# Kernel tuning notes

Measured on AMD Instinct MI355X. Metric: run time of the kernel, lower is better.

The kernel has to match this reference:

```python
import jax, jax.numpy as jnp
import numpy as np
import math

B, L, D = 8, 2048, 256


def setup_inputs() -> dict:
    key = jax.random.key(0)
    ks = jax.random.split(key, 8)
    return {
        "query": jax.random.normal(ks[0], (B, L, D), dtype=jnp.float32),
        "key": jax.random.normal(ks[1], (B, L, D), dtype=jnp.float32),
        "value": jax.random.normal(ks[2], (B, L, D), dtype=jnp.float32),
        "mask": jax.random.randint(ks[3], (B, L), 0, 2, dtype=jnp.int32),
        "Wq_w": jax.random.normal(ks[4], (D, D), dtype=jnp.float32) * 0.05,
        "Wq_b": jax.random.normal(ks[5], (D,), dtype=jnp.float32) * 0.05,
        "Wk_w": jax.random.normal(ks[6], (D, D), dtype=jnp.float32) * 0.05,
        "Wk_b": jax.random.normal(ks[7], (D,), dtype=jnp.float32) * 0.05,
    }


def reference(query, key, value, mask, Wq_w, Wq_b, Wk_w, Wk_b):
    d = query.shape[-1]
    q = query @ Wq_w.T + Wq_b            # [B, Lq, D]
    k = key @ Wk_w.T + Wk_b              # [B, Lk, D]
    scores = jnp.einsum("bqd,bkd->bqk", q, k) / math.sqrt(d)  # [B, Lq, Lk]
    m = mask.astype(scores.dtype)[:, None, :]                  # [B, 1, Lk]
    # multiplicative then additive masking, as in original
    scores = jnp.where(m == 0, jnp.asarray(-1e9, scores.dtype), scores * m)
    attn = jax.nn.softmax(scores, axis=-1)
    return jnp.einsum("bqk,bkd->bqd", attn, value)
```

## Files before the change

### kernel.cpp

```cpp
#include <hip/hip_runtime.h>
#include <stdint.h>
#include <stddef.h>

#define B_ 8
#define L_ 2048
#define D_ 256
#define KSPLIT 4
#define KRANGE 512
#define KTILE 32
#define NITER 16
#define PSS 40

typedef __bf16 bf16x8 __attribute__((ext_vector_type(8)));
typedef float floatx4 __attribute__((ext_vector_type(4)));
typedef _Float16 half4_t __attribute__((ext_vector_type(4)));

__device__ __forceinline__ short f2bf(float f) {
    union { float f; uint32_t u; } v; v.f = f;
    return (short)((v.u + 0x8000u) >> 16);
}

__device__ __forceinline__ uint32_t pack2bf(float a, float b) {
    union { float f; uint32_t u; } x, y; x.f = a; y.f = b;
    return ((x.u + 0x8000u) >> 16) | ((y.u + 0x8000u) & 0xFFFF0000u);
}

__device__ __forceinline__ void async16(const void* g, void* l) {
    __builtin_amdgcn_global_load_lds(
        (__attribute__((address_space(1))) void*)g,
        (__attribute__((address_space(3))) void*)l,
        16, 0, 0);
}

__global__ __launch_bounds__(256, 3) void proj_kernel(
    const float* __restrict__ Xq, const float* __restrict__ Xk,
    const float* __restrict__ Wq, const float* __restrict__ Wk,
    const float* __restrict__ bq, const float* __restrict__ bk,
    short* __restrict__ Oq, short* __restrict__ Ok)
{
    const float* X    = blockIdx.y ? Xk : Xq;
    const float* W    = blockIdx.y ? Wk : Wq;
    const float* bias = blockIdx.y ? bk : bq;
    short* Out        = blockIdx.y ? Ok : Oq;

    __shared__ uint32_t As[2][64 * 20];
    __shared__ uint32_t Ws[2][256 * 20];

    const int tid  = threadIdx.x;
    const int wid  = tid >> 6;
    const int lane = tid & 63;
    const int m16  = lane & 15;
    const int quad = lane >> 4;
    const int row0 = blockIdx.x * 64;
    const int ar = tid >> 2, cg = tid & 3;

    floatx4 acc[16];
    const floatx4 z4 = {0.f, 0.f, 0.f, 0.f};
#pragma unroll
    for (int i = 0; i < 16; i++) acc[i] = z4;

    {
        const float* srcA = X + (size_t)(row0 + ar) * D_ + cg * 8;
        float4 a = *(const float4*)srcA, b2 = *(const float4*)(srcA + 4);
        uint4 u; u.x = pack2bf(a.x, a.y); u.y = pack2bf(a.z, a.w);
        u.z = pack2bf(b2.x, b2.y); u.w = pack2bf(b2.z, b2.w);
        *(uint4*)&As[0][ar * 20 + cg * 4] = u;
#pragma unroll
        for (int p = 0; p < 4; p++) {
            const float* srcW = W + (size_t)(p * 64 + ar) * D_ + cg * 8;
            float4 wa = *(const float4*)srcW, wb = *(const float4*)(srcW + 4);
            uint4 w; w.x = pack2bf(wa.x, wa.y); w.y = pack2bf(wa.z, wa.w);
            w.z = pack2bf(wb.x, wb.y); w.w = pack2bf(wb.z, wb.w);
            *(uint4*)&Ws[0][(p * 64 + ar) * 20 + cg * 4] = w;
        }
    }
    __syncthreads();

    for (int kc = 0; kc < 8; kc++) {
        const int buf = kc & 1;
        float4 na, nb, nwa[4], nwb[4];
        if (kc < 7) {
            const int k1 = (kc + 1) * 32;
            const float* srcA = X + (size_t)(row0 + ar) * D_ + k1 + cg * 8;
            na = *(const float4*)srcA; nb = *(const float4*)(srcA + 4);
#pragma unroll
            for (int p = 0; p < 4; p++) {
                const float* srcW = W + (size_t)(p * 64 + ar) * D_ + k1 + cg * 8;
                nwa[p] = *(const float4*)srcW; nwb[p] = *(const float4*)(srcW + 4);
            }
        }
        bf16x8 af = *(const bf16x8*)&As[buf][(wid * 16 + m16) * 20 + quad * 4];
#pragma unroll
        for (int n = 0; n < 16; n++) {
            bf16x8 bfr = *(const bf16x8*)&Ws[buf][(n * 16 + m16) * 20 + quad * 4];
            acc[n] = __builtin_amdgcn_mfma_f32_16x16x32_bf16(af, bfr, acc[n], 0, 0, 0);
        }
        if (kc < 7) {
            uint4 u; u.x = pack2bf(na.x, na.y); u.y = pack2bf(na.z, na.w);
            u.z = pack2bf(nb.x, nb.y); u.w = pack2bf(nb.z, nb.w);
            *(uint4*)&As[buf ^ 1][ar * 20 + cg * 4] = u;
#pragma unroll
            for (int p = 0; p < 4; p++) {
                uint4 w; w.x = pack2bf(nwa[p].x, nwa[p].y); w.y = pack2bf(nwa[p].z, nwa[p].w);
                w.z = pack2bf(nwb[p].x, nwb[p].y); w.w = pack2bf(nwb[p].z, nwb[p].w);
                *(uint4*)&Ws[buf ^ 1][(p * 64 + ar) * 20 + cg * 4] = w;
            }
        }
        __syncthreads();
    }
#pragma unroll
    for (int n = 0; n < 16; n++) {
        const int col = n * 16 + m16;
        const float bv = bias[col];
#pragma unroll
        for (int r = 0; r < 4; r++) {
            const int row = row0 + wid * 16 + quad * 4 + r;
            Out[(size_t)row * D_ + col] = f2bf(acc[n][r] + bv);
        }
    }
}

__global__ __launch_bounds__(256, 2) void vtrans_kernel(
    const float* __restrict__ V, short* __restrict__ Vt)
{
    __shared__ uint32_t T[256 * 20];
    const int tid = threadIdx.x;
    const int b  = blockIdx.y;
    const int l0 = blockIdx.x * 32;
    const int r2 = tid >> 4;
    const int dg = tid & 15;
    const int lp = r2 ^ ((dg & 3) << 2);
#pragma unroll
    for (int p = 0; p < 4; p++) {
        int d0 = (dg + p * 16) * 4;
        const float* src = V + ((size_t)b * L_ + l0 + r2 * 2) * D_ + d0;
        float4 e0 = *(const float4*)src;
        float4 e1 = *(const float4*)(src + D_);
        T[(d0 + 0) * 20 + lp] = pack2bf(e0.x, e1.x);
        T[(d0 + 1) * 20 + lp] = pack2bf(e0.y, e1.y);
        T[(d0 + 2) * 20 + lp] = pack2bf(e0.z, e1.z);
        T[(d0 + 3) * 20 + lp] = pack2bf(e0.w, e1.w);
    }
    __syncthreads();
#pragma unroll
    for (int p = 0; p < 4; p++) {
        int d = (tid >> 2) + p * 64;
        int c = tid & 3;
        int cp = c ^ ((d >> 2) & 3);
        uint4 u = *(const uint4*)&T[d * 20 + cp * 4];
        *(uint4*)(Vt + ((size_t)b * D_ + d) * L_ + l0 + c * 8) = u;
    }
}

__global__ __launch_bounds__(256, 2) void flash_kernel(
    const short* __restrict__ Qb, const short* __restrict__ Kb,
    const short* __restrict__ Vt, const int* __restrict__ mask,
    float* __restrict__ Out, _Float16* __restrict__ Part,
    float* __restrict__ Lpart)
{
    __shared__ short Ks[2][KTILE * 256];
    __shared__ short Vs[2][256 * KTILE];
    __shared__ short Ps[4 * 32 * PSS];

    const int tid  = threadIdx.x;
    const int wid  = tid >> 6;
    const int lane = tid & 63;
    const int m16  = lane & 15;
    const int quad = lane >> 4;
    const int b  = blockIdx.x;
    const int q0 = blockIdx.y * 128;
    const int z  = blockIdx.z;

    const short* kbase = Kb + ((size_t)b * L_ + z * KRANGE) * D_;
    const short* vbase = Vt + (size_t)b * D_ * L_;
    const int*   mg    = mask + b * L_ + z * KRANGE;

    bf16x8 qf[2][8];
    {
        const short* qrow = Qb + ((size_t)b * L_ + q0 + wid * 32) * D_;
#pragma unroll
        for (int s2 = 0; s2 < 2; s2++)
#pragma unroll
            for (int kk = 0; kk < 8; kk++)
                qf[s2][kk] = *(const bf16x8*)(qrow + (size_t)(s2 * 16 + m16) * D_ + kk * 32 + quad * 8);
    }

    floatx4 o[2][16];
    const floatx4 z4 = {0.f, 0.f, 0.f, 0.f};
#pragma unroll
    for (int s2 = 0; s2 < 2; s2++)
#pragma unroll
        for (int n = 0; n < 16; n++) o[s2][n] = z4;
    float rsum[2][4] = {{0.f,0.f,0.f,0.f},{0.f,0.f,0.f,0.f}};

    auto stageK = [&](int t, int bufi) {
        short* kl = &Ks[bufi][0];
#pragma unroll
        for (int c = 0; c < 4; c++) {
            int unit = wid * 4 + c;
            int row = unit * 2 + (lane >> 5);
            int g = (lane & 31) ^ (row & 7);
            async16(kbase + (size_t)(t * KTILE + row) * D_ + g * 8, kl + unit * 512);
        }
    };
    auto stageV = [&](int t, int bufi) {
        short* vl = &Vs[bufi][0];
#pragma unroll
        for (int c = 0; c < 4; c++) {
            int unit = wid * 4 + c;
            int d = unit * 16 + (lane >> 2);
            int g = (lane & 3) ^ ((lane >> 2) & 3);
            async16(vbase + (size_t)d * L_ + z * KRANGE + t * KTILE + g * 8, vl + unit * 512);
        }
    };

    stageK(0, 0);
    __builtin_amdgcn_s_waitcnt(0x0F70);
    __syncthreads();

    short* ps = Ps + wid * (32 * PSS);
    const float C2 = 0.09016844f;
    bf16x8 pf0, pf1;

    for (int t = 0; t < NITER; t++) {
        const int buf = t & 1;
        if (t + 1 < NITER) stageK(t + 1, buf ^ 1);
        stageV(t, buf);
        const short* kl = &Ks[buf][0];

        int mv0 = mg[t * KTILE + m16];
        int mv1 = mg[t * KTILE + 16 + m16];

        floatx4 sA[2][2];
#pragma unroll
        for (int s2 = 0; s2 < 2; s2++) { sA[s2][0] = z4; sA[s2][1] = z4; }
#pragma unroll
        for (int kk = 0; kk < 8; kk++) {
#pragma unroll
            for (int j = 0; j < 2; j++) {
                int row = j * 16 + m16;
                int cidx = (kk * 4 + quad) ^ (m16 & 7);
                bf16x8 kf = *(const bf16x8*)(kl + row * 256 + cidx * 8);
                sA[0][j] = __builtin_amdgcn_mfma_f32_16x16x32_bf16(qf[0][kk], kf, sA[0][j], 0, 0, 0);
                sA[1][j] = __builtin_amdgcn_mfma_f32_16x16x32_bf16(qf[1][kk], kf, sA[1][j], 0, 0, 0);
            }
        }

        if (t > 0) {
            const short* vl = &Vs[buf ^ 1][0];
#pragma unroll
            for (int n = 0; n < 16; n++) {
                int rowd = n * 16 + m16;
                int cidx = quad ^ (m16 & 3);
                bf16x8 vf = *(const bf16x8*)(vl + rowd * 32 + cidx * 8);
                o[0][n] = __builtin_amdgcn_mfma_f32_16x16x32_bf16(pf0, vf, o[0][n], 0, 0, 0);
                o[1][n] = __builtin_amdgcn_mfma_f32_16x16x32_bf16(pf1, vf, o[1][n], 0, 0, 0);
            }
        }

        float moff0 = mv0 ? 0.f : -1.0e30f;
        float moff1 = mv1 ? 0.f : -1.0e30f;
#pragma unroll
        for (int s2 = 0; s2 < 2; s2++) {
#pragma unroll
            for (int j = 0; j < 2; j++) {
                const float moff = j ? moff1 : moff0;
#pragma unroll
                for (int r = 0; r < 4; r++) {
                    float p = exp2f(fmaf(sA[s2][j][r], C2, moff));
                    rsum[s2][r] += p;
                    ps[(s2 * 16 + quad * 4 + r) * PSS + j * 16 + m16] = f2bf(p);
                }
            }
        }
        __builtin_amdgcn_s_waitcnt(0xC07F);
        pf0 = *(const bf16x8*)(ps + (size_t)m16 * PSS + quad * 8);
        pf1 = *(const bf16x8*)(ps + (size_t)(16 + m16) * PSS + quad * 8);

        __builtin_amdgcn_s_waitcnt(0x0F70);
        __syncthreads();
    }

    {
        const short* vl = &Vs[(NITER - 1) & 1][0];
#pragma unroll
        for (int n = 0; n < 16; n++) {
            int rowd = n * 16 + m16;
            int cidx = quad ^ (m16 & 3);
            bf16x8 vf = *(const bf16x8*)(vl + rowd * 32 + cidx * 8);
            o[0][n] = __builtin_amdgcn_mfma_f32_16x16x32_bf16(pf0, vf, o[0][n], 0, 0, 0);
            o[1][n] = __builtin_amdgcn_mfma_f32_16x16x32_bf16(pf1, vf, o[1][n], 0, 0, 0);
        }
    }

#pragma unroll
    for (int s2 = 0; s2 < 2; s2++)
#pragma unroll
        for (int r = 0; r < 4; r++) {
            float x = rsum[s2][r];
            x += __shfl_xor(x, 1, 16);
            x += __shfl_xor(x, 2, 16);
            x += __shfl_xor(x, 4, 16);
            x += __shfl_xor(x, 8, 16);
            rsum[s2][r] = x;
        }

    const size_t BLD = (size_t)B_ * L_ * D_;
    const size_t rowbase = (size_t)b * L_ + q0 + wid * 32;
    if (z == 0) {
        float* po = Out + rowbase * D_;
#pragma unroll
        for (int s2 = 0; s2 < 2; s2++)
#pragma unroll
            for (int n = 0; n < 16; n++)
#pragma unroll
                for (int r = 0; r < 4; r++)
                    po[(size_t)(s2 * 16 + quad * 4 + r) * D_ + n * 16 + m16] = o[s2][n][r];
    } else {
        _Float16* pp = Part + (size_t)(z - 1) * BLD + rowbase * D_;
#pragma unroll
        for (int s2 = 0; s2 < 2; s2++)
#pragma unroll
            for (int n = 0; n < 16; n++)
#pragma unroll
                for (int r = 0; r < 4; r++)
                    pp[(size_t)(s2 * 16 + quad * 4 + r) * D_ + n * 16 + m16] = (_Float16)o[s2][n][r];
    }
    if (m16 == 0) {
#pragma unroll
        for (int s2 = 0; s2 < 2; s2++)
#pragma unroll
            for (int r = 0; r < 4; r++)
                Lpart[(size_t)z * (B_ * L_) + rowbase + s2 * 16 + quad * 4 + r] = rsum[s2][r];
    }
}

__global__ __launch_bounds__(256) void norm_kernel(
    float* __restrict__ Out, const _Float16* __restrict__ Part,
    const float* __restrict__ Lpart)
{
    const int idx = blockIdx.x * 256 + threadIdx.x;
    const int row = idx >> 6;
    const int c   = (idx & 63) * 4;
    const size_t off = (size_t)row * D_ + c;
    const size_t BLD = (size_t)B_ * L_ * D_;
    float4 acc = *(float4*)(Out + off);
#pragma unroll
    for (int zz = 0; zz < 3; zz++) {
        half4_t h = *(const half4_t*)(Part + zz * BLD + off);
        acc.x += (float)h.x; acc.y += (float)h.y;
        acc.z += (float)h.z; acc.w += (float)h.w;
    }
    const int BL = B_ * L_;
    float l = Lpart[row] + Lpart[BL + row] + Lpart[2 * BL + row] + Lpart[3 * BL + row];
    float inv = 1.0f / l;
    acc.x *= inv; acc.y *= inv; acc.z *= inv; acc.w *= inv;
    *(float4*)(Out + off) = acc;
}

extern "C" void kernel_launch(void* const* d_in, const int* in_sizes, int n_in,
                              void* d_out, int out_size, void* d_ws, size_t ws_size,
                              hipStream_t stream) {
    const float* query = (const float*)d_in[0];
    const float* key   = (const float*)d_in[1];
    const float* value = (const float*)d_in[2];
    const int*   mask  = (const int*)d_in[3];
    const float* Wq_w  = (const float*)d_in[4];
    const float* Wq_b  = (const float*)d_in[5];
    const float* Wk_w  = (const float*)d_in[6];
    const float* Wk_b  = (const float*)d_in[7];
    float* out = (float*)d_out;

    const size_t BLD = (size_t)B_ * L_ * D_;
    short* qb = (short*)d_ws;
    short* kb = qb + BLD;
    short* vt = kb + BLD;
    _Float16* part = (_Float16*)(vt + BLD);
    float* lpart = (float*)(part + 3 * BLD);

    proj_kernel<<<dim3(256, 2), 256, 0, stream>>>(query, key, Wq_w, Wk_w, Wq_b, Wk_b, qb, kb);
    vtrans_kernel<<<dim3(64, 8), 256, 0, stream>>>(value, vt);
    flash_kernel<<<dim3(8, 16, 4), 256, 0, stream>>>(qb, kb, vt, mask, out, part, lpart);
    norm_kernel<<<dim3((B_ * L_ * D_ / 4) / 256), 256, 0, stream>>>(out, part, lpart);
}
```

Measured before the change: 188.9 us.

## Shrink flash tiles to 16 query rows per wave and raise occupancy

Halves each wave's query tile to 16 rows and the K tile to 16 keys. The grid doubles along the query axis and launch bounds now request four blocks per CU. V is staged in a single 32-key buffer refreshed every other iteration, and P·V runs on odd iterations, replacing the previous software-pipelined double-buffered V. This aims to raise occupancy and cut register pressure, at the cost of loading K/V twice as often per query and of more barriers and iterations.

```diff
diff --git a/kernel.cpp b/kernel.cpp
--- a/kernel.cpp
+++ b/kernel.cpp
@@ -7,8 +7,8 @@
 #define D_ 256
 #define KSPLIT 4
 #define KRANGE 512
-#define KTILE 32
-#define NITER 16
+#define KTILE 16
+#define NITER 32
 #define PSS 40
 
 typedef __bf16 bf16x8 __attribute__((ext_vector_type(8)));
@@ -152,15 +152,15 @@
     }
 }
 
-__global__ __launch_bounds__(256, 2) void flash_kernel(
+__global__ __launch_bounds__(256, 4) void flash_kernel(
     const short* __restrict__ Qb, const short* __restrict__ Kb,
     const short* __restrict__ Vt, const int* __restrict__ mask,
     float* __restrict__ Out, _Float16* __restrict__ Part,
     float* __restrict__ Lpart)
 {
     __shared__ short Ks[2][KTILE * 256];
-    __shared__ short Vs[2][256 * KTILE];
-    __shared__ short Ps[4 * 32 * PSS];
+    __shared__ short Vs[256 * 32];
+    __shared__ short Ps[4 * 16 * PSS];
 
     const int tid  = threadIdx.x;
     const int wid  = tid >> 6;
@@ -168,170 +168,126 @@
     const int m16  = lane & 15;
     const int quad = lane >> 4;
     const int b  = blockIdx.x;
-    const int q0 = blockIdx.y * 128;
+    const int q0 = blockIdx.y * 64;
     const int z  = blockIdx.z;
 
     const short* kbase = Kb + ((size_t)b * L_ + z * KRANGE) * D_;
-    const short* vbase = Vt + (size_t)b * D_ * L_;
+    const short* vbase = Vt + (size_t)b * D_ * L_ + z * KRANGE;
     const int*   mg    = mask + b * L_ + z * KRANGE;
 
-    bf16x8 qf[2][8];
+    bf16x8 qf[8];
     {
-        const short* qrow = Qb + ((size_t)b * L_ + q0 + wid * 32) * D_;
-#pragma unroll
-        for (int s2 = 0; s2 < 2; s2++)
-#pragma unroll
-            for (int kk = 0; kk < 8; kk++)
-                qf[s2][kk] = *(const bf16x8*)(qrow + (size_t)(s2 * 16 + m16) * D_ + kk * 32 + quad * 8);
-    }
-
-    floatx4 o[2][16];
+        const short* qrow = Qb + ((size_t)b * L_ + q0 + wid * 16 + m16) * D_;
+#pragma unroll
+        for (int kk = 0; kk < 8; kk++)
+            qf[kk] = *(const bf16x8*)(qrow + kk * 32 + quad * 8);
+    }
+
+    floatx4 o[16];
     const floatx4 z4 = {0.f, 0.f, 0.f, 0.f};
 #pragma unroll
-    for (int s2 = 0; s2 < 2; s2++)
-#pragma unroll
-        for (int n = 0; n < 16; n++) o[s2][n] = z4;
-    float rsum[2][4] = {{0.f,0.f,0.f,0.f},{0.f,0.f,0.f,0.f}};
+    for (int n = 0; n < 16; n++) o[n] = z4;
+    float rsum[4] = {0.f, 0.f, 0.f, 0.f};
 
     auto stageK = [&](int t, int bufi) {
-        short* kl = &Ks[bufi][0];
+#pragma unroll
+        for (int c = 0; c < 2; c++) {
+            int rbase = wid * 4 + c * 2;
+            int row = rbase + (lane >> 5);
+            int g = (lane & 31) ^ (row & 7);
+            async16(kbase + (size_t)(t * KTILE + row) * D_ + g * 8,
+                    &Ks[bufi][rbase * 256]);
+        }
+    };
+    auto stageV = [&](int P) {
 #pragma unroll
         for (int c = 0; c < 4; c++) {
-            int unit = wid * 4 + c;
-            int row = unit * 2 + (lane >> 5);
-            int g = (lane & 31) ^ (row & 7);
-            async16(kbase + (size_t)(t * KTILE + row) * D_ + g * 8, kl + unit * 512);
+            int rbase = wid * 64 + c * 16;
+            int d = rbase + (lane >> 2);
+            int g = (lane & 3) ^ (d & 3) ^ ((d >> 2) & 3);
+            async16(vbase + (size_t)d * L_ + P * 32 + g * 8, &Vs[rbase * 32]);
         }
     };
-    auto stageV = [&](int t, int bufi) {
-        short* vl = &Vs[bufi][0];
-#pragma unroll
-        for (int c = 0; c < 4; c++) {
-            int unit = wid * 4 + c;
-            int d = unit * 16 + (lane >> 2);
-            int g = (lane & 3) ^ ((lane >> 2) & 3);
-            async16(vbase + (size_t)d * L_ + z * KRANGE + t * KTILE + g * 8, vl + unit * 512);
-        }
-    };
 
     stageK(0, 0);
+    stageV(0);
     __builtin_amdgcn_s_waitcnt(0x0F70);
     __syncthreads();
 
-    short* ps = Ps + wid * (32 * PSS);
+    short* ps = Ps + wid * (16 * PSS);
     const float C2 = 0.09016844f;
-    bf16x8 pf0, pf1;
 
     for (int t = 0; t < NITER; t++) {
         const int buf = t & 1;
         if (t + 1 < NITER) stageK(t + 1, buf ^ 1);
-        stageV(t, buf);
+        if (t > 0 && (t & 1) == 0) stageV(t >> 1);
+
         const short* kl = &Ks[buf][0];
-
-        int mv0 = mg[t * KTILE + m16];
-        int mv1 = mg[t * KTILE + 16 + m16];
-
-        floatx4 sA[2][2];
-#pragma unroll
-        for (int s2 = 0; s2 < 2; s2++) { sA[s2][0] = z4; sA[s2][1] = z4; }
+        floatx4 s = z4;
 #pragma unroll
         for (int kk = 0; kk < 8; kk++) {
-#pragma unroll
-            for (int j = 0; j < 2; j++) {
-                int row = j * 16 + m16;
-                int cidx = (kk * 4 + quad) ^ (m16 & 7);
-                bf16x8 kf = *(const bf16x8*)(kl + row * 256 + cidx * 8);
-                sA[0][j] = __builtin_amdgcn_mfma_f32_16x16x32_bf16(qf[0][kk], kf, sA[0][j], 0, 0, 0);
-                sA[1][j] = __builtin_amdgcn_mfma_f32_16x16x32_bf16(qf[1][kk], kf, sA[1][j], 0, 0, 0);
+            int cidx = (kk * 4 + quad) ^ (m16 & 7);
+            bf16x8 kf = *(const bf16x8*)(kl + m16 * 256 + cidx * 8);
+            s = __builtin_amdgcn_mfma_f32_16x16x32_bf16(qf[kk], kf, s, 0, 0, 0);
+        }
+
+        const int mv = mg[t * KTILE + m16];
+        const float moff = mv ? 0.f : -1.0e30f;
+        const int ph = (t & 1) * 16;
+#pragma unroll
+        for (int r = 0; r < 4; r++) {
+            float p = exp2f(fmaf(s[r], C2, moff));
+            rsum[r] += p;
+            ps[(quad * 4 + r) * PSS + ph + m16] = f2bf(p);
+        }
+
+        if (t & 1) {
+            __builtin_amdgcn_s_waitcnt(0xC07F);
+            bf16x8 pf = *(const bf16x8*)(ps + m16 * PSS + quad * 8);
+#pragma unroll
+            for (int n = 0; n < 16; n++) {
+                int d = n * 16 + m16;
+                int cidx = quad ^ (d & 3) ^ ((d >> 2) & 3);
+                bf16x8 vf = *(const bf16x8*)(Vs + d * 32 + cidx * 8);
+                o[n] = __builtin_amdgcn_mfma_f32_16x16x32_bf16(pf, vf, o[n], 0, 0, 0);
             }
         }
-
-        if (t > 0) {
-            const short* vl = &Vs[buf ^ 1][0];
-#pragma unroll
-            for (int n = 0; n < 16; n++) {
-                int rowd = n * 16 + m16;
-                int cidx = quad ^ (m16 & 3);
-                bf16x8 vf = *(const bf16x8*)(vl + rowd * 32 + cidx * 8);
-                o[0][n] = __builtin_amdgcn_mfma_f32_16x16x32_bf16(pf0, vf, o[0][n], 0, 0, 0);
-                o[1][n] = __builtin_amdgcn_mfma_f32_16x16x32_bf16(pf1, vf, o[1][n], 0, 0, 0);
-            }
-        }
-
-        float moff0 = mv0 ? 0.f : -1.0e30f;
-        float moff1 = mv1 ? 0.f : -1.0e30f;
-#pragma unroll
-        for (int s2 = 0; s2 < 2; s2++) {
-#pragma unroll
-            for (int j = 0; j < 2; j++) {
-                const float moff = j ? moff1 : moff0;
-#pragma unroll
-                for (int r = 0; r < 4; r++) {
-                    float p = exp2f(fmaf(sA[s2][j][r], C2, moff));
-                    rsum[s2][r] += p;
-                    ps[(s2 * 16 + quad * 4 + r) * PSS + j * 16 + m16] = f2bf(p);
-                }
-            }
-        }
-        __builtin_amdgcn_s_waitcnt(0xC07F);
-        pf0 = *(const bf16x8*)(ps + (size_t)m16 * PSS + quad * 8);
-        pf1 = *(const bf16x8*)(ps + (size_t)(16 + m16) * PSS + quad * 8);
 
         __builtin_amdgcn_s_waitcnt(0x0F70);
         __syncthreads();
     }
 
-    {
-        const short* vl = &Vs[(NITER - 1) & 1][0];
-#pragma unroll
-        for (int n = 0; n < 16; n++) {
-            int rowd = n * 16 + m16;
-            int cidx = quad ^ (m16 & 3);
-            bf16x8 vf = *(const bf16x8*)(vl + rowd * 32 + cidx * 8);
-            o[0][n] = __builtin_amdgcn_mfma_f32_16x16x32_bf16(pf0, vf, o[0][n], 0, 0, 0);
-            o[1][n] = __builtin_amdgcn_mfma_f32_16x16x32_bf16(pf1, vf, o[1][n], 0, 0, 0);
-        }
-    }
-
-#pragma unroll
-    for (int s2 = 0; s2 < 2; s2++)
-#pragma unroll
-        for (int r = 0; r < 4; r++) {
-            float x = rsum[s2][r];
-            x += __shfl_xor(x, 1, 16);
-            x += __shfl_xor(x, 2, 16);
-            x += __shfl_xor(x, 4, 16);
-            x += __shfl_xor(x, 8, 16);
-            rsum[s2][r] = x;
-        }
+#pragma unroll
+    for (int r = 0; r < 4; r++) {
+        float x = rsum[r];
+        x += __shfl_xor(x, 1, 16);
+        x += __shfl_xor(x, 2, 16);
+        x += __shfl_xor(x, 4, 16);
+        x += __shfl_xor(x, 8, 16);
+        rsum[r] = x;
+    }
 
     const size_t BLD = (size_t)B_ * L_ * D_;
-    const size_t rowbase = (size_t)b * L_ + q0 + wid * 32;
+    const size_t rowbase = (size_t)b * L_ + q0 + wid * 16;
     if (z == 0) {
         float* po = Out + rowbase * D_;
 #pragma unroll
-        for (int s2 = 0; s2 < 2; s2++)
-#pragma unroll
-            for (int n = 0; n < 16; n++)
-#pragma unroll
-                for (int r = 0; r < 4; r++)
-                    po[(size_t)(s2 * 16 + quad * 4 + r) * D_ + n * 16 + m16] = o[s2][n][r];
+        for (int n = 0; n < 16; n++)
+#pragma unroll
+            for (int r = 0; r < 4; r++)
+                po[(size_t)(quad * 4 + r) * D_ + n * 16 + m16] = o[n][r];
     } else {
         _Float16* pp = Part + (size_t)(z - 1) * BLD + rowbase * D_;
 #pragma unroll
-        for (int s2 = 0; s2 < 2; s2++)
-#pragma unroll
-            for (int n = 0; n < 16; n++)
-#pragma unroll
-                for (int r = 0; r < 4; r++)
-                    pp[(size_t)(s2 * 16 + quad * 4 + r) * D_ + n * 16 + m16] = (_Float16)o[s2][n][r];
+        for (int n = 0; n < 16; n++)
+#pragma unroll
+            for (int r = 0; r < 4; r++)
+                pp[(size_t)(quad * 4 + r) * D_ + n * 16 + m16] = (_Float16)o[n][r];
     }
     if (m16 == 0) {
 #pragma unroll
-        for (int s2 = 0; s2 < 2; s2++)
-#pragma unroll
-            for (int r = 0; r < 4; r++)
-                Lpart[(size_t)z * (B_ * L_) + rowbase + s2 * 16 + quad * 4 + r] = rsum[s2][r];
+        for (int r = 0; r < 4; r++)
+            Lpart[(size_t)z * (B_ * L_) + rowbase + quad * 4 + r] = rsum[r];
     }
 }
 
@@ -380,6 +336,6 @@
 
     proj_kernel<<<dim3(256, 2), 256, 0, stream>>>(query, key, Wq_w, Wk_w, Wq_b, Wk_b, qb, kb);
     vtrans_kernel<<<dim3(64, 8), 256, 0, stream>>>(value, vt);
-    flash_kernel<<<dim3(8, 16, 4), 256, 0, stream>>>(qb, kb, vt, mask, out, part, lpart);
+    flash_kernel<<<dim3(8, 32, 4), 256, 0, stream>>>(qb, kb, vt, mask, out, part, lpart);
     norm_kernel<<<dim3((B_ * L_ * D_ / 4) / 256), 256, 0, stream>>>(out, part, lpart);
 }
```

Result: slower. 263.3 us (+39.4%).
